# Performance work log

Hardware: AMD Instinct MI355X
Metric: run time of the kernel (lower is better)

Reference implementation:

```python
import jax, jax.numpy as jnp
import numpy as np

TAU = 1.0
EPS = 1e-8  # F.cosine_similarity eps


def _cl(X, Y):
    # Pairwise cosine similarity via L2-normalize + single GEMM (N,D)@(D,N)
    Xn = X / jnp.maximum(jnp.linalg.norm(X, axis=1, keepdims=True), EPS)
    Yn = Y / jnp.maximum(jnp.linalg.norm(Y, axis=1, keepdims=True), EPS)
    sim = Xn @ Yn.T  # [N, N], sim[i, j] = cos(X_i, Y_j)
    e = jnp.exp(sim / TAU)
    pos = jnp.diagonal(e)               # exp(diag(sim)/tau), [N]
    neg = jnp.sum(e, axis=0) - pos      # column sums minus positive, [N]
    return -jnp.log(pos / neg).reshape(X.shape[0], 1)


def setup_inputs() -> dict:
    key = jax.random.key(0)
    ks = jax.random.split(key, 6)
    N, D1, D2, DO = 8192, 1024, 768, 256
    X = jax.random.normal(ks[0], (N, D1), dtype=jnp.float32)
    Y = jax.random.normal(ks[1], (N, D2), dtype=jnp.float32)
    # nn.Linear params (kaiming-uniform-ish scale)
    Wx = jax.random.uniform(ks[2], (DO, D1), jnp.float32, -1, 1) / np.sqrt(D1)
    bx = jax.random.uniform(ks[3], (DO,), jnp.float32, -1, 1) / np.sqrt(D1)
    Wy = jax.random.uniform(ks[4], (DO, D2), jnp.float32, -1, 1) / np.sqrt(D2)
    by = jax.random.uniform(ks[5], (DO,), jnp.float32, -1, 1) / np.sqrt(D2)
    return {"X": X, "Y": Y, "Wx": Wx, "bx": bx, "Wy": Wy, "by": by}


def reference(X, Y, Wx, bx, Wy, by):
    Xp = X @ Wx.T + bx  # proj_x
    Yp = Y @ Wy.T + by  # proj_y
    return _cl(Xp, Yp) + _cl(Yp, Xp)  # [N, 1]
```

## Files before the change

kernel.cpp:

```cpp
#include <hip/hip_runtime.h>
#include <hip/hip_bf16.h>

typedef __bf16 bf16_t;
typedef __bf16 bf16x8 __attribute__((ext_vector_type(8)));
typedef float  f32x4  __attribute__((ext_vector_type(4)));
typedef int    i32x8  __attribute__((ext_vector_type(8)));

__device__ __forceinline__ bf16x8 pack8(f32x4 a, f32x4 b) {
    bf16x8 h = { (bf16_t)a.x, (bf16_t)a.y, (bf16_t)a.z, (bf16_t)a.w,
                 (bf16_t)b.x, (bf16_t)b.y, (bf16_t)b.z, (bf16_t)b.w };
    return h;
}

__device__ __forceinline__ void gl_lds16(const void* g, void* l) {
    __builtin_amdgcn_global_load_lds(
        (const __attribute__((address_space(1))) unsigned int*)g,
        (__attribute__((address_space(3))) unsigned int*)l, 16, 0, 0);
}

#if __has_builtin(__builtin_amdgcn_cvt_pk_fp8_f32)
__device__ __forceinline__ unsigned char cvt1_e4m3(float x) {
    return (unsigned char)(__builtin_amdgcn_cvt_pk_fp8_f32(x, x, 0, false) & 0xff);
}
#else
__device__ __forceinline__ unsigned char cvt1_e4m3(float x) {
    unsigned u = __float_as_uint(x);
    unsigned sign = (u >> 24) & 0x80u;
    float a = fabsf(x);
    if (a < 7.8125e-3f) { int q = (int)(a * 512.0f + 0.5f); return (unsigned char)(sign | q); }
    if (a >= 448.0f) return (unsigned char)(sign | 0x7E);
    unsigned au = u & 0x7FFFFFFFu;
    unsigned lsb = (au >> 20) & 1u;
    au += 0x7FFFFu + lsb;
    int exp = (int)(au >> 23) - 127;
    unsigned man = (au >> 20) & 7u;
    return (unsigned char)(sign | ((unsigned)(exp + 7) << 3) | man);
}
#endif

__device__ __forceinline__ int frag_off_k(int row16, int k) {
    return ((k >> 6) << 10) + (((k >> 3) & 3) << 8) + (row16 << 4)
         + (((k >> 5) & 1) << 3) + (k & 7);
}

__global__ __launch_bounds__(256) void wconv(
    const float* __restrict__ Wx, const float* __restrict__ Wy,
    bf16_t* __restrict__ Wxt, bf16_t* __restrict__ Wyt,
    float* __restrict__ sums)
{
    int id = blockIdx.x * 256 + threadIdx.x;
    if (blockIdx.x < 64) sums[id] = 0.0f;

    int row, k0, K;
    const float* W;
    bf16_t* Wt;
    if (id < 32768) { W = Wx; Wt = Wxt; K = 1024; row = id >> 7; k0 = (id & 127) << 3; }
    else { int c = id - 32768; W = Wy; Wt = Wyt; K = 768; row = c / 96; k0 = (c % 96) << 3; }

    f32x4 lo = *reinterpret_cast<const f32x4*>(&W[(size_t)row * K + k0]);
    f32x4 hi = *reinterpret_cast<const f32x4*>(&W[(size_t)row * K + k0 + 4]);
    size_t off = (size_t)(row >> 4) * 16 * K + frag_off_k(row & 15, k0);
    *reinterpret_cast<bf16x8*>(Wt + off) = pack8(lo, hi);
}

__global__ __launch_bounds__(256, 4) void proj_norm(
    const float* __restrict__ X, const float* __restrict__ Y,
    const bf16_t* __restrict__ Wxt, const float* __restrict__ bxp,
    const bf16_t* __restrict__ Wyt, const float* __restrict__ byp,
    unsigned char* __restrict__ Xt, unsigned char* __restrict__ Yt)
{
    __shared__ float Abuf[2][32 * 64];
    __shared__ unsigned char obuf[8192];
    __shared__ float ssqL[4][32];

    const int tid  = threadIdx.x;
    const int lane = tid & 63;
    const int wave = tid >> 6;
    const int quad = lane >> 4;
    const int c16  = lane & 15;
    const int cg   = wave;

    const bool isY = blockIdx.x >= 256;
    const float*  A    = isY ? Y   : X;
    const bf16_t* Wt   = isY ? Wyt : Wxt;
    const float*  bias = isY ? byp : bxp;
    unsigned char* dst = isY ? Yt  : Xt;
    const int K = isY ? 768 : 1024;
    const int S = K >> 6;
    const int rowBase = (blockIdx.x & 255) * 32;

    auto stage = [&](int s, int b) {
        #pragma unroll
        for (int t = 0; t < 2; ++t) {
            int r0  = (wave * 2 + t) * 4;
            int row = r0 + (lane >> 4);
            int gch = (lane & 15) ^ (row & 15);
            gl_lds16(&A[(size_t)(rowBase + row) * K + s * 64 + gch * 4],
                     &Abuf[b][r0 * 64]);
        }
    };

    auto aFrag = [&](int b, int mf, int s2) -> bf16x8 {
        int row = mf * 16 + c16;
        int e   = s2 * 8 + quad * 2;
        const float* base = &Abuf[b][row * 64];
        f32x4 lo = *reinterpret_cast<const f32x4*>(base + ((e ^ c16) << 2));
        f32x4 hi = *reinterpret_cast<const f32x4*>(base + (((e + 1) ^ c16) << 2));
        return pack8(lo, hi);
    };

    const bf16_t* pB[4];
    #pragma unroll
    for (int nf = 0; nf < 4; ++nf)
        pB[nf] = Wt + (size_t)(cg * 4 + nf) * 16 * K + quad * 256 + c16 * 16;

    f32x4 acc[2][4] = {};
    stage(0, 0);

    for (int s = 0; s < S; ++s) {
        const int b = s & 1;
        __syncthreads();
        if (s + 1 < S) stage(s + 1, b ^ 1);
        #pragma unroll
        for (int s2 = 0; s2 < 2; ++s2) {
            bf16x8 bF[4];
            #pragma unroll
            for (int nf = 0; nf < 4; ++nf)
                bF[nf] = *reinterpret_cast<const bf16x8*>(pB[nf] + s * 1024 + s2 * 8);
            #pragma unroll
            for (int mf = 0; mf < 2; ++mf) {
                bf16x8 aF = aFrag(b, mf, s2);
                #pragma unroll
                for (int nf = 0; nf < 4; ++nf)
                    acc[mf][nf] = __builtin_amdgcn_mfma_f32_16x16x32_bf16(
                        aF, bF[nf], acc[mf][nf], 0, 0, 0);
            }
        }
    }

    #pragma unroll
    for (int nf = 0; nf < 4; ++nf) {
        float bb = bias[cg * 64 + nf * 16 + c16];
        #pragma unroll
        for (int mf = 0; mf < 2; ++mf)
            #pragma unroll
            for (int r = 0; r < 4; ++r) acc[mf][nf][r] += bb;
    }

    #pragma unroll
    for (int mf = 0; mf < 2; ++mf)
        #pragma unroll
        for (int r = 0; r < 4; ++r) {
            float v = 0.f;
            #pragma unroll
            for (int nf = 0; nf < 4; ++nf) v += acc[mf][nf][r] * acc[mf][nf][r];
            v += __shfl_xor(v, 1, 64);
            v += __shfl_xor(v, 2, 64);
            v += __shfl_xor(v, 4, 64);
            v += __shfl_xor(v, 8, 64);
            if (c16 == 0) ssqL[cg][mf * 16 + quad * 4 + r] = v;
        }
    __syncthreads();

    #pragma unroll
    for (int mf = 0; mf < 2; ++mf)
        #pragma unroll
        for (int r = 0; r < 4; ++r) {
            int lr = mf * 16 + quad * 4 + r;
            float t = ssqL[0][lr] + ssqL[1][lr] + ssqL[2][lr] + ssqL[3][lr];
            float inv = 1.0f / fmaxf(sqrtf(t), 1e-8f);
            #pragma unroll
            for (int nf = 0; nf < 4; ++nf) {
                int k = cg * 64 + nf * 16 + c16;
                obuf[((lr >> 4) << 12) + ((k >> 5) << 9) + ((lr & 15) << 5) + (k & 31)] =
                    cvt1_e4m3(acc[mf][nf][r] * inv);
            }
        }
    __syncthreads();

    const f32x4* src = reinterpret_cast<const f32x4*>(&obuf[tid * 32]);
    f32x4* g = reinterpret_cast<f32x4*>(dst + (size_t)rowBase * 256 + tid * 32);
    g[0] = src[0];
    g[1] = src[1];
}

__global__ __launch_bounds__(256, 2) void sim_gemm(
    const unsigned char* __restrict__ Xt, const unsigned char* __restrict__ Yt,
    float* __restrict__ rowsum, float* __restrict__ colsum,
    float* __restrict__ pos)
{
    __shared__ float red2[2][128];

    const int tid  = threadIdx.x;
    const int lane = tid & 63;
    const int wave = tid >> 6;
    const int quad = lane >> 4;
    const int c16  = lane & 15;
    const int wy   = wave >> 1;
    const int wx   = wave & 1;

    const int id = blockIdx.x;
    const int b2 = id >> 3;
    const int colBlk = (id & 7) * 8 + (b2 >> 4);
    const int rowGrp = b2 & 15;
    const int colBase = colBlk * 128;

    i32x8 B0[4], B1[4];
    #pragma unroll
    for (int nf = 0; nf < 4; ++nf) {
        const i32x8* p = reinterpret_cast<const i32x8*>(
            Yt + (size_t)(colBase + wx * 64 + nf * 16) * 256 + quad * 512 + c16 * 32);
        B0[nf] = p[0];
        B1[nf] = p[64];
    }

    auto aPtr = [&](int rowBase, int mf) {
        return reinterpret_cast<const i32x8*>(
            Xt + (size_t)(rowBase + wy * 64 + mf * 16) * 256 + quad * 512 + c16 * 32);
    };

    i32x8 A0[4], A1[4];
    #pragma unroll
    for (int mf = 0; mf < 4; ++mf) {
        const i32x8* p = aPtr(rowGrp * 512, mf);
        A0[mf] = p[0];
        A1[mf] = p[64];
    }

    float cs[4] = {0.f, 0.f, 0.f, 0.f};

    for (int t = 0; t < 4; ++t) {
        const int rowBase = rowGrp * 512 + t * 128;

        f32x4 acc[4][4] = {};
        #pragma unroll
        for (int mf = 0; mf < 4; ++mf)
            #pragma unroll
            for (int nf = 0; nf < 4; ++nf)
                acc[mf][nf] = __builtin_amdgcn_mfma_scale_f32_16x16x128_f8f6f4(
                    A0[mf], B0[nf], acc[mf][nf], 0, 0, 0, 127, 0, 127);
        #pragma unroll
        for (int mf = 0; mf < 4; ++mf)
            #pragma unroll
            for (int nf = 0; nf < 4; ++nf)
                acc[mf][nf] = __builtin_amdgcn_mfma_scale_f32_16x16x128_f8f6f4(
                    A1[mf], B1[nf], acc[mf][nf], 0, 0, 0, 127, 0, 127);

        if (t < 3) {
            #pragma unroll
            for (int mf = 0; mf < 4; ++mf) {
                const i32x8* p = aPtr(rowBase + 128, mf);
                A0[mf] = p[0];
                A1[mf] = p[64];
            }
        }

        #pragma unroll
        for (int mf = 0; mf < 4; ++mf)
            #pragma unroll
            for (int nf = 0; nf < 4; ++nf)
                #pragma unroll
                for (int r = 0; r < 4; ++r)
                    acc[mf][nf][r] = __expf(acc[mf][nf][r]);

        if (rowBase == colBase) {
            #pragma unroll
            for (int mf = 0; mf < 4; ++mf)
                #pragma unroll
                for (int nf = 0; nf < 4; ++nf)
                    #pragma unroll
                    for (int r = 0; r < 4; ++r) {
                        int lrow = wy * 64 + mf * 16 + quad * 4 + r;
                        int lcol = wx * 64 + nf * 16 + c16;
                        if (lrow == lcol) pos[rowBase + lrow] = acc[mf][nf][r];
                    }
        }

        float rs[4][4];
        #pragma unroll
        for (int mf = 0; mf < 4; ++mf)
            #pragma unroll
            for (int r = 0; r < 4; ++r) {
                float v = acc[mf][0][r] + acc[mf][1][r] + acc[mf][2][r] + acc[mf][3][r];
                v += __shfl_xor(v, 1, 64);
                v += __shfl_xor(v, 2, 64);
                v += __shfl_xor(v, 4, 64);
                v += __shfl_xor(v, 8, 64);
                rs[mf][r] = v;
            }

        #pragma unroll
        for (int nf = 0; nf < 4; ++nf) {
            float v = 0.f;
            #pragma unroll
            for (int mf = 0; mf < 4; ++mf)
                #pragma unroll
                for (int r = 0; r < 4; ++r)
                    v += acc[mf][nf][r];
            cs[nf] += v;
        }

        __syncthreads();
        if (c16 == 0) {
            #pragma unroll
            for (int mf = 0; mf < 4; ++mf)
                #pragma unroll
                for (int r = 0; r < 4; ++r)
                    red2[wx][wy * 64 + mf * 16 + quad * 4 + r] = rs[mf][r];
        }
        __syncthreads();
        if (tid < 128)
            atomicAdd(&rowsum[rowBase + tid], red2[0][tid] + red2[1][tid]);
    }

    float csr[4];
    #pragma unroll
    for (int nf = 0; nf < 4; ++nf) {
        float v = cs[nf];
        v += __shfl_xor(v, 16, 64);
        v += __shfl_xor(v, 32, 64);
        csr[nf] = v;
    }
    __syncthreads();
    if (quad == 0) {
        #pragma unroll
        for (int nf = 0; nf < 4; ++nf)
            red2[wy][wx * 64 + nf * 16 + c16] = csr[nf];
    }
    __syncthreads();
    if (tid < 128)
        atomicAdd(&colsum[colBase + tid], red2[0][tid] + red2[1][tid]);
}

__global__ __launch_bounds__(256) void finalize(
    const float* __restrict__ rowsum, const float* __restrict__ colsum,
    const float* __restrict__ pos, float* __restrict__ out)
{
    int i = blockIdx.x * 256 + threadIdx.x;
    float p = pos[i];
    out[i] = logf(colsum[i] - p) + logf(rowsum[i] - p) - 2.0f * logf(p);
}

extern "C" void kernel_launch(void* const* d_in, const int* in_sizes, int n_in,
                              void* d_out, int out_size, void* d_ws, size_t ws_size,
                              hipStream_t stream) {
    const float* X  = (const float*)d_in[0];
    const float* Y  = (const float*)d_in[1];
    const float* Wx = (const float*)d_in[2];
    const float* bx = (const float*)d_in[3];
    const float* Wy = (const float*)d_in[4];
    const float* by = (const float*)d_in[5];
    float* out = (float*)d_out;

    char* ws = (char*)d_ws;
    unsigned char* Xt  = (unsigned char*)(ws);
    unsigned char* Yt  = (unsigned char*)(ws + (2u << 20));
    bf16_t*        Wxt = (bf16_t*)(ws + (4u << 20));
    bf16_t*        Wyt = (bf16_t*)(ws + (4u << 20) + (512u << 10));
    float* rowsum = (float*)(ws + (5u << 20));
    float* colsum = rowsum + 8192;
    float* pos    = colsum + 8192;

    wconv<<<224, 256, 0, stream>>>(Wx, Wy, Wxt, Wyt, rowsum);
    proj_norm<<<512, 256, 0, stream>>>(X, Y, Wxt, bx, Wyt, by, Xt, Yt);
    sim_gemm<<<1024, 256, 0, stream>>>(Xt, Yt, rowsum, colsum, pos);
    finalize<<<32, 256, 0, stream>>>(rowsum, colsum, pos, out);
}
```

Measured before the change: 154.3 us.

## Halve sim_gemm column tile and replace atomics with partial-sum buffers

```diff
diff --git a/kernel.cpp b/kernel.cpp
--- a/kernel.cpp
+++ b/kernel.cpp
@@ -45,11 +45,9 @@
 
 __global__ __launch_bounds__(256) void wconv(
     const float* __restrict__ Wx, const float* __restrict__ Wy,
-    bf16_t* __restrict__ Wxt, bf16_t* __restrict__ Wyt,
-    float* __restrict__ sums)
+    bf16_t* __restrict__ Wxt, bf16_t* __restrict__ Wyt)
 {
     int id = blockIdx.x * 256 + threadIdx.x;
-    if (blockIdx.x < 64) sums[id] = 0.0f;
 
     int row, k0, K;
     const float* W;
@@ -184,9 +182,9 @@
     g[1] = src[1];
 }
 
-__global__ __launch_bounds__(256, 2) void sim_gemm(
+__global__ __launch_bounds__(256, 3) void sim_gemm(
     const unsigned char* __restrict__ Xt, const unsigned char* __restrict__ Yt,
-    float* __restrict__ rowsum, float* __restrict__ colsum,
+    float* __restrict__ rowsumP, float* __restrict__ colsumP,
     float* __restrict__ pos)
 {
     __shared__ float red2[2][128];
@@ -201,15 +199,15 @@
 
     const int id = blockIdx.x;
     const int b2 = id >> 3;
-    const int colBlk = (id & 7) * 8 + (b2 >> 4);
+    const int colBlk = (id & 7) * 16 + (b2 >> 4);
     const int rowGrp = b2 & 15;
-    const int colBase = colBlk * 128;
-
-    i32x8 B0[4], B1[4];
-    #pragma unroll
-    for (int nf = 0; nf < 4; ++nf) {
+    const int colBase = colBlk * 64;
+
+    i32x8 B0[2], B1[2];
+    #pragma unroll
+    for (int nf = 0; nf < 2; ++nf) {
         const i32x8* p = reinterpret_cast<const i32x8*>(
-            Yt + (size_t)(colBase + wx * 64 + nf * 16) * 256 + quad * 512 + c16 * 32);
+            Yt + (size_t)(colBase + wx * 32 + nf * 16) * 256 + quad * 512 + c16 * 32);
         B0[nf] = p[0];
         B1[nf] = p[64];
     }
@@ -227,22 +225,22 @@
         A1[mf] = p[64];
     }
 
-    float cs[4] = {0.f, 0.f, 0.f, 0.f};
+    float cs[2] = {0.f, 0.f};
 
     for (int t = 0; t < 4; ++t) {
         const int rowBase = rowGrp * 512 + t * 128;
 
-        f32x4 acc[4][4] = {};
+        f32x4 acc[4][2] = {};
         #pragma unroll
         for (int mf = 0; mf < 4; ++mf)
             #pragma unroll
-            for (int nf = 0; nf < 4; ++nf)
+            for (int nf = 0; nf < 2; ++nf)
                 acc[mf][nf] = __builtin_amdgcn_mfma_scale_f32_16x16x128_f8f6f4(
                     A0[mf], B0[nf], acc[mf][nf], 0, 0, 0, 127, 0, 127);
         #pragma unroll
         for (int mf = 0; mf < 4; ++mf)
             #pragma unroll
-            for (int nf = 0; nf < 4; ++nf)
+            for (int nf = 0; nf < 2; ++nf)
                 acc[mf][nf] = __builtin_amdgcn_mfma_scale_f32_16x16x128_f8f6f4(
                     A1[mf], B1[nf], acc[mf][nf], 0, 0, 0, 127, 0, 127);
 
@@ -258,21 +256,22 @@
         #pragma unroll
         for (int mf = 0; mf < 4; ++mf)
             #pragma unroll
-            for (int nf = 0; nf < 4; ++nf)
+            for (int nf = 0; nf < 2; ++nf)
                 #pragma unroll
                 for (int r = 0; r < 4; ++r)
                     acc[mf][nf][r] = __expf(acc[mf][nf][r]);
 
-        if (rowBase == colBase) {
+        const int d = colBase - rowBase;
+        if (d == 0 || d == 64) {
             #pragma unroll
             for (int mf = 0; mf < 4; ++mf)
                 #pragma unroll
-                for (int nf = 0; nf < 4; ++nf)
+                for (int nf = 0; nf < 2; ++nf)
                     #pragma unroll
                     for (int r = 0; r < 4; ++r) {
                         int lrow = wy * 64 + mf * 16 + quad * 4 + r;
-                        int lcol = wx * 64 + nf * 16 + c16;
-                        if (lrow == lcol) pos[rowBase + lrow] = acc[mf][nf][r];
+                        int lcol = wx * 32 + nf * 16 + c16;
+                        if (lrow == d + lcol) pos[rowBase + lrow] = acc[mf][nf][r];
                     }
         }
 
@@ -281,7 +280,7 @@
         for (int mf = 0; mf < 4; ++mf)
             #pragma unroll
             for (int r = 0; r < 4; ++r) {
-                float v = acc[mf][0][r] + acc[mf][1][r] + acc[mf][2][r] + acc[mf][3][r];
+                float v = acc[mf][0][r] + acc[mf][1][r];
                 v += __shfl_xor(v, 1, 64);
                 v += __shfl_xor(v, 2, 64);
                 v += __shfl_xor(v, 4, 64);
@@ -290,7 +289,7 @@
             }
 
         #pragma unroll
-        for (int nf = 0; nf < 4; ++nf) {
+        for (int nf = 0; nf < 2; ++nf) {
             float v = 0.f;
             #pragma unroll
             for (int mf = 0; mf < 4; ++mf)
@@ -310,35 +309,63 @@
         }
         __syncthreads();
         if (tid < 128)
-            atomicAdd(&rowsum[rowBase + tid], red2[0][tid] + red2[1][tid]);
-    }
-
-    float csr[4];
-    #pragma unroll
-    for (int nf = 0; nf < 4; ++nf) {
+            rowsumP[(size_t)colBlk * 8192 + rowBase + tid] =
+                red2[0][tid] + red2[1][tid];
+    }
+
+    #pragma unroll
+    for (int nf = 0; nf < 2; ++nf) {
         float v = cs[nf];
         v += __shfl_xor(v, 16, 64);
         v += __shfl_xor(v, 32, 64);
-        csr[nf] = v;
+        cs[nf] = v;
     }
     __syncthreads();
     if (quad == 0) {
         #pragma unroll
-        for (int nf = 0; nf < 4; ++nf)
-            red2[wy][wx * 64 + nf * 16 + c16] = csr[nf];
-    }
-    __syncthreads();
-    if (tid < 128)
-        atomicAdd(&colsum[colBase + tid], red2[0][tid] + red2[1][tid]);
+        for (int nf = 0; nf < 2; ++nf)
+            red2[wy][wx * 32 + nf * 16 + c16] = cs[nf];
+    }
+    __syncthreads();
+    if (tid < 64)
+        colsumP[(size_t)rowGrp * 8192 + colBase + tid] =
+            red2[0][tid] + red2[1][tid];
 }
 
 __global__ __launch_bounds__(256) void finalize(
-    const float* __restrict__ rowsum, const float* __restrict__ colsum,
+    const float* __restrict__ rowsumP, const float* __restrict__ colsumP,
     const float* __restrict__ pos, float* __restrict__ out)
 {
-    int i = blockIdx.x * 256 + threadIdx.x;
-    float p = pos[i];
-    out[i] = logf(colsum[i] - p) + logf(rowsum[i] - p) - 2.0f * logf(p);
+    __shared__ float redR[256], redC[256];
+
+    const int oi   = threadIdx.x & 31;
+    const int part = threadIdx.x >> 5;
+    const int i    = blockIdx.x * 32 + oi;
+
+    float r = 0.f;
+    #pragma unroll
+    for (int c = part; c < 128; c += 8)
+        r += rowsumP[(size_t)c * 8192 + i];
+
+    float cv = 0.f;
+    #pragma unroll
+    for (int g = part; g < 16; g += 8)
+        cv += colsumP[(size_t)g * 8192 + i];
+
+    redR[threadIdx.x] = r;
+    redC[threadIdx.x] = cv;
+    __syncthreads();
+
+    if (threadIdx.x < 32) {
+        float rsum = 0.f, csum = 0.f;
+        #pragma unroll
+        for (int p = 0; p < 8; ++p) {
+            rsum += redR[oi + 32 * p];
+            csum += redC[oi + 32 * p];
+        }
+        float p = pos[i];
+        out[i] = logf(csum - p) + logf(rsum - p) - 2.0f * logf(p);
+    }
 }
 
 extern "C" void kernel_launch(void* const* d_in, const int* in_sizes, int n_in,
@@ -357,12 +384,12 @@
     unsigned char* Yt  = (unsigned char*)(ws + (2u << 20));
     bf16_t*        Wxt = (bf16_t*)(ws + (4u << 20));
     bf16_t*        Wyt = (bf16_t*)(ws + (4u << 20) + (512u << 10));
-    float* rowsum = (float*)(ws + (5u << 20));
-    float* colsum = rowsum + 8192;
-    float* pos    = colsum + 8192;
-
-    wconv<<<224, 256, 0, stream>>>(Wx, Wy, Wxt, Wyt, rowsum);
+    float* rowsumP = (float*)(ws + (5u << 20));
+    float* colsumP = (float*)(ws + (9u << 20));
+    float* pos     = (float*)(ws + (10u << 20));
+
+    wconv<<<224, 256, 0, stream>>>(Wx, Wy, Wxt, Wyt);
     proj_norm<<<512, 256, 0, stream>>>(X, Y, Wxt, bx, Wyt, by, Xt, Yt);
-    sim_gemm<<<1024, 256, 0, stream>>>(Xt, Yt, rowsum, colsum, pos);
-    finalize<<<32, 256, 0, stream>>>(rowsum, colsum, pos, out);
-}
+    sim_gemm<<<2048, 256, 0, stream>>>(Xt, Yt, rowsumP, colsumP, pos);
+    finalize<<<256, 256, 0, stream>>>(rowsumP, colsumP, pos, out);
+}
```

Measured after the change: 212.3 us. +37.6%, slower.
